# Kernel optimization log

Hardware: AMD Instinct MI355X
Metric: run time of the kernel (lower is better)

Reference implementation:

```python
import jax, jax.numpy as jnp
import numpy as np

DK, DV, NH = 512, 256, 8  # matches init_kwargs


def rel_to_abs(x):
    # x: (B, N, L, 2L-1) -> (B, N, L, L) via pad/reshape trick
    B, N, L, _ = x.shape
    x = jnp.pad(x, ((0, 0), (0, 0), (0, 0), (0, 1)))          # (B,N,L,2L)
    x = x.reshape(B, N, L * 2 * L)
    x = jnp.pad(x, ((0, 0), (0, 0), (0, L - 1)))
    x = x.reshape(B, N, L + 1, 2 * L - 1)
    return x[:, :, :L, L - 1:]


def relative_logits_1d(q, rel_k):
    # q: (B, nh, A, Wd, dkh); rel_k: (dkh, 2*Wd-1)
    B, nh, A, Wd, _ = q.shape
    rel = jnp.einsum('bnawc,cm->bnawm', q, rel_k)             # (B,nh,A,Wd,2Wd-1)
    rel = rel.reshape(B, nh * A, Wd, 2 * Wd - 1)
    rel = rel_to_abs(rel).reshape(B, nh, A, 1, Wd, Wd)
    return jnp.broadcast_to(rel, (B, nh, A, A, Wd, Wd))


def reference(x, w_qkv, w_conv, w_out, key_rel_h, key_rel_w):
    B, Cin, H, W = x.shape
    dkh, dvh = DK // NH, DV // NH
    L = H * W
    # 1x1 qkv projection (stride 1)
    qkv = jnp.einsum('bchw,oc->bohw', x, w_qkv)               # (B, 2dk+dv, H, W)
    q = qkv[:, :DK]
    k = qkv[:, DK:2 * DK]
    v = qkv[:, 2 * DK:]
    flat_q = q.reshape(B, NH, dkh, L) * (dkh ** -0.5)
    flat_k = k.reshape(B, NH, dkh, L)
    flat_v = v.reshape(B, NH, dvh, L)
    logits = jnp.einsum('bncs,bnct->bnst', flat_q, flat_k)     # (B,nh,L,L)
    # relative position logits (uses the already-scaled q, as in the torch code)
    qr = flat_q.reshape(B, NH, dkh, H, W).transpose(0, 1, 3, 4, 2)  # (B,nh,H,W,dkh)
    w_rel = relative_logits_1d(qr, key_rel_w)                  # (B,nh,H,H,W,W)
    h_rel = relative_logits_1d(qr.transpose(0, 1, 3, 2, 4), key_rel_h)  # (B,nh,W,W,H,H)
    h_rel = h_rel.transpose(0, 1, 2, 4, 3, 5).reshape(B, NH, L, L)
    w_rel = w_rel.transpose(0, 1, 4, 2, 5, 3).reshape(B, NH, L, L)
    logits = logits + h_rel + w_rel
    weights = jax.nn.softmax(logits, axis=-1)
    attn = jnp.einsum('bnst,bnct->bnsc', weights, flat_v)      # (B,nh,L,dvh)
    attn = attn.transpose(0, 1, 3, 2).reshape(B, DV, H, W)
    attn = jnp.einsum('bchw,oc->bohw', attn, w_out)            # 1x1 out_proj
    conv_out = jax.lax.conv_general_dilated(
        x, w_conv, window_strides=(1, 1), padding=[(1, 1), (1, 1)],
        dimension_numbers=('NCHW', 'OIHW', 'NCHW'))            # (B, out_c-dv, H, W)
    return jnp.concatenate([conv_out, attn], axis=1)


def setup_inputs() -> dict:
    key = jax.random.key(0)
    ks = jax.random.split(key, 6)
    H, W, Cin = 32, 32, 256
    return {
        'x': jax.random.normal(ks[0], (8, Cin, H, W), jnp.float32),
        'w_qkv': jax.random.normal(ks[1], (2 * DK + DV, Cin), jnp.float32) * 0.02,
        'w_conv': jax.random.normal(ks[2], (256, Cin, 3, 3), jnp.float32) * 0.02,
        'w_out': jax.random.normal(ks[3], (DV, DV), jnp.float32) * 0.02,
        'key_rel_h': DK ** -0.5 + jax.random.normal(ks[4], (DK // NH, 2 * H - 1), jnp.float32),
        'key_rel_w': DK ** -0.5 + jax.random.normal(ks[5], (DK // NH, 2 * W - 1), jnp.float32),
    }
```

## Files before the change

kernel.cpp:

```cpp
#include <hip/hip_runtime.h>
#include <cstddef>
#include <cstdint>

#define NB 8
#define CIN 256
#define LL 1024
#define DKC 512
#define DVC 256
#define XPSTRIDE 295936

typedef short short8 __attribute__((ext_vector_type(8)));
typedef float f32x4 __attribute__((ext_vector_type(4)));

__device__ __forceinline__ unsigned short f2bf(float f) {
  unsigned int u = __float_as_uint(f);
  u += 0x7fffu + ((u >> 16) & 1u);
  return (unsigned short)(u >> 16);
}
__device__ __forceinline__ float bf2f(unsigned short u) {
  return __uint_as_float(((unsigned int)u) << 16);
}

__global__ __launch_bounds__(256) void prep_weights(
    const float* __restrict__ wconv, const float* __restrict__ wqkv,
    const float* __restrict__ wout, const float* __restrict__ krh,
    const float* __restrict__ krw, unsigned short* __restrict__ wtap,
    unsigned short* __restrict__ wqbf, unsigned short* __restrict__ woutbf,
    unsigned short* __restrict__ relTh, unsigned short* __restrict__ relTw) {
  const int idx = blockIdx.x * 256 + threadIdx.x;
  if (idx < 589824) {
    const int tap = idx >> 16;
    const int rem = idx & 65535;
    wtap[idx] = f2bf(wconv[(size_t)rem * 9 + tap]);
  } else if (idx < 917504) {
    const int j = idx - 589824;
    const int o = j >> 8;
    const float sc = (o < DKC) ? 0.125f * 1.44269504088896f : 1.0f;
    wqbf[j] = f2bf(wqkv[j] * sc);
  } else if (idx < 983040) {
    const int j = idx - 917504;
    woutbf[j] = f2bf(wout[j]);
  } else {
    const int j = idx - 983040;
    const int tbl = j >> 12;
    const int rest = j & 4095;
    const int m = rest >> 6, c = rest & 63;
    const float* src = tbl ? krw : krh;
    unsigned short* dst = tbl ? relTw : relTh;
    const float v = (m < 63) ? src[c * 63 + m] : 0.f;
    dst[m * 64 + c] = f2bf(v);
  }
}

__global__ __launch_bounds__(256) void xpad_border(unsigned short* __restrict__ xTp) {
  const int idx = blockIdx.x * 256 + threadIdx.x;
  const int b = idx / 33792;
  const int rem = idx - b * 33792;
  const int pos = rem >> 8, c = rem & 255;
  int hp, wp;
  if (pos < 34) { hp = 0; wp = pos; }
  else if (pos < 68) { hp = 33; wp = pos - 34; }
  else if (pos < 100) { hp = pos - 68 + 1; wp = 0; }
  else { hp = pos - 100 + 1; wp = 33; }
  xTp[(size_t)b * XPSTRIDE + (hp * 34 + wp) * 256 + c] = 0;
}

__global__ __launch_bounds__(256) void xpad_interior(
    const float* __restrict__ x, unsigned short* __restrict__ xTp) {
  __shared__ float tile[64][65];
  const int st = blockIdx.x;
  const int b = blockIdx.y;
  const int s0 = st * 64;
  const int h0 = st * 2;
  const int tid = threadIdx.x;
  for (int cc = 0; cc < 4; ++cc) {
    const int c0 = cc * 64;
    {
      const int row = tid >> 2;
      const int j0 = (tid & 3) * 16;
#pragma unroll
      for (int k = 0; k < 4; ++k)
        *(float4*)&tile[row][j0 + k * 4] =
            *(const float4*)(x + ((size_t)(b * CIN + c0 + row)) * LL + s0 + j0 + k * 4);
    }
    __syncthreads();
    {
      const int sl = tid >> 2;
      const int cb = (tid & 3) * 16;
      unsigned short buf[16];
#pragma unroll
      for (int m = 0; m < 16; ++m) buf[m] = f2bf(tile[cb + m][sl]);
      const int hp = h0 + (sl >> 5) + 1;
      const int wp = (sl & 31) + 1;
      unsigned short* dst = xTp + (size_t)b * XPSTRIDE + (hp * 34 + wp) * 256 + c0 + cb;
      *(uint4*)dst = *(uint4*)&buf[0];
      *(uint4*)(dst + 8) = *(uint4*)&buf[8];
    }
    __syncthreads();
  }
}

__global__ __launch_bounds__(256) void qkv_mfma(
    const unsigned short* __restrict__ xTp, const unsigned short* __restrict__ wqbf,
    unsigned short* __restrict__ qbf, unsigned short* __restrict__ kbf,
    unsigned short* __restrict__ vbf) {
  __shared__ __align__(16) unsigned short as[64 * 64];
  __shared__ __align__(16) unsigned short bs[64 * 64];
  __shared__ float trans[64][65];
  const int tid = threadIdx.x;
  const int lane = tid & 63, w = tid >> 6;
  const int n16 = lane & 15, quad = lane >> 4;
  const int ot = blockIdx.x;
  const int st = blockIdx.y;
  const int b = blockIdx.z;
  const int o0 = ot * 64;
  const int s0 = st * 64;
  const int h0 = st * 2;
  const int trow = tid >> 3, ck = tid & 7;

  const unsigned short* xb = xTp + (size_t)b * XPSTRIDE;
  const unsigned short* wt = wqbf + (size_t)o0 * 256;
  const int wpos = (trow & 31) + 1;

  f32x4 acc[4];
#pragma unroll
  for (int nt = 0; nt < 4; ++nt) acc[nt] = (f32x4){0.f, 0.f, 0.f, 0.f};

  uint4 ra0, ra1, rb0, rb1;
  {
    ra0 = *(const uint4*)(wt + (size_t)trow * 256 + ck * 8);
    ra1 = *(const uint4*)(wt + (size_t)(trow + 32) * 256 + ck * 8);
    rb0 = *(const uint4*)(xb + (size_t)((h0 + 1) * 34 + wpos) * 256 + ck * 8);
    rb1 = *(const uint4*)(xb + (size_t)((h0 + 2) * 34 + wpos) * 256 + ck * 8);
  }
#pragma unroll
  for (int kc = 0; kc < 4; ++kc) {
    __syncthreads();
    *(uint4*)&as[trow * 64 + ((ck ^ (trow & 7)) * 8)] = ra0;
    *(uint4*)&as[(trow + 32) * 64 + ((ck ^ (trow & 7)) * 8)] = ra1;
    *(uint4*)&bs[trow * 64 + ((ck ^ (trow & 7)) * 8)] = rb0;
    *(uint4*)&bs[(trow + 32) * 64 + ((ck ^ (trow & 7)) * 8)] = rb1;
    __syncthreads();
    if (kc < 3) {
      const int c0 = (kc + 1) * 64;
      ra0 = *(const uint4*)(wt + (size_t)trow * 256 + c0 + ck * 8);
      ra1 = *(const uint4*)(wt + (size_t)(trow + 32) * 256 + c0 + ck * 8);
      rb0 = *(const uint4*)(xb + (size_t)((h0 + 1) * 34 + wpos) * 256 + c0 + ck * 8);
      rb1 = *(const uint4*)(xb + (size_t)((h0 + 2) * 34 + wpos) * 256 + c0 + ck * 8);
    }
    short8 a0 = *(const short8*)&as[(w * 16 + n16) * 64 + ((quad ^ (n16 & 7)) * 8)];
    short8 a1 = *(const short8*)&as[(w * 16 + n16) * 64 + (((quad + 4) ^ (n16 & 7)) * 8)];
#pragma unroll
    for (int nt = 0; nt < 4; ++nt) {
      short8 b0 = *(const short8*)&bs[(nt * 16 + n16) * 64 + ((quad ^ (n16 & 7)) * 8)];
      short8 b1 = *(const short8*)&bs[(nt * 16 + n16) * 64 + (((quad + 4) ^ (n16 & 7)) * 8)];
      acc[nt] = __builtin_amdgcn_mfma_f32_16x16x32_bf16(a0, b0, acc[nt], 0, 0, 0);
      acc[nt] = __builtin_amdgcn_mfma_f32_16x16x32_bf16(a1, b1, acc[nt], 0, 0, 0);
    }
  }
  __syncthreads();
#pragma unroll
  for (int nt = 0; nt < 4; ++nt)
#pragma unroll
    for (int reg = 0; reg < 4; ++reg)
      trans[w * 16 + quad * 4 + reg][nt * 16 + n16] = acc[nt][reg];
  __syncthreads();
  const int sl = tid >> 2;
  const int cseg = (tid & 3) * 16;
  unsigned short buf[16];
  if (ot < 16) {
#pragma unroll
    for (int m = 0; m < 16; ++m) buf[m] = f2bf(trans[cseg + m][sl]);
    unsigned short* dst;
    int head;
    if (ot < 8) { dst = qbf; head = ot; }
    else { dst = kbf; head = ot - 8; }
    const size_t base = (((size_t)(b * 8 + head)) * LL + s0 + sl) * 64 + cseg;
    *(uint4*)(dst + base) = *(uint4*)&buf[0];
    *(uint4*)(dst + base + 8) = *(uint4*)&buf[8];
  } else {
#pragma unroll
    for (int m = 0; m < 16; ++m) buf[m] = f2bf(trans[sl][cseg + m]);
    unsigned short* dst = vbf + ((size_t)b * DVC + (ot - 16) * 64 + sl) * LL + s0 + cseg;
    *(uint4*)dst = *(uint4*)&buf[0];
    *(uint4*)(dst + 8) = *(uint4*)&buf[8];
  }
}

__global__ __launch_bounds__(256) void conv_mfma(
    const unsigned short* __restrict__ xTp, const unsigned short* __restrict__ wtap,
    float* __restrict__ out) {
  __shared__ __align__(16) unsigned short as[64 * 64];
  __shared__ __align__(16) unsigned short bs[64 * 64];
  const int tid = threadIdx.x;
  const int lane = tid & 63, w = tid >> 6;
  const int n16 = lane & 15, quad = lane >> 4;
  const int ot = blockIdx.x;
  const int st = blockIdx.y;
  const int b = blockIdx.z;
  const int s0 = st * 64;
  const int h0 = st * 2;
  const int trow = tid >> 3;
  const int ck = tid & 7;

  const unsigned short* xb = xTp + (size_t)b * XPSTRIDE;
  const unsigned short* wbase = wtap + (size_t)(ot * 64) * 256;

  f32x4 acc[4];
#pragma unroll
  for (int nt = 0; nt < 4; ++nt) acc[nt] = (f32x4){0.f, 0.f, 0.f, 0.f};

  uint4 ra0, ra1, rb0, rb1;
  auto loadtile = [&](int it) {
    const int tap = it >> 2;
    const int c0 = (it & 3) * 64;
    const int dh = tap / 3 - 1;
    const int dw = tap - (tap / 3) * 3 - 1;
    const unsigned short* wt = wbase + (size_t)tap * 65536;
    ra0 = *(const uint4*)(wt + (size_t)trow * 256 + c0 + ck * 8);
    ra1 = *(const uint4*)(wt + (size_t)(trow + 32) * 256 + c0 + ck * 8);
    const int wp = (trow & 31) + dw + 1;
    rb0 = *(const uint4*)(xb + (size_t)((h0 + dh + 1) * 34 + wp) * 256 + c0 + ck * 8);
    rb1 = *(const uint4*)(xb + (size_t)((h0 + dh + 2) * 34 + wp) * 256 + c0 + ck * 8);
  };
  loadtile(0);
  for (int it = 0; it < 36; ++it) {
    __syncthreads();
    *(uint4*)&as[trow * 64 + ((ck ^ (trow & 7)) * 8)] = ra0;
    *(uint4*)&as[(trow + 32) * 64 + ((ck ^ (trow & 7)) * 8)] = ra1;
    *(uint4*)&bs[trow * 64 + ((ck ^ (trow & 7)) * 8)] = rb0;
    *(uint4*)&bs[(trow + 32) * 64 + ((ck ^ (trow & 7)) * 8)] = rb1;
    __syncthreads();
    if (it < 35) loadtile(it + 1);
    short8 a0 = *(const short8*)&as[(w * 16 + n16) * 64 + ((quad ^ (n16 & 7)) * 8)];
    short8 a1 = *(const short8*)&as[(w * 16 + n16) * 64 + (((quad + 4) ^ (n16 & 7)) * 8)];
#pragma unroll
    for (int nt = 0; nt < 4; ++nt) {
      short8 b0 = *(const short8*)&bs[(nt * 16 + n16) * 64 + ((quad ^ (n16 & 7)) * 8)];
      short8 b1 = *(const short8*)&bs[(nt * 16 + n16) * 64 + (((quad + 4) ^ (n16 & 7)) * 8)];
      acc[nt] = __builtin_amdgcn_mfma_f32_16x16x32_bf16(a0, b0, acc[nt], 0, 0, 0);
      acc[nt] = __builtin_amdgcn_mfma_f32_16x16x32_bf16(a1, b1, acc[nt], 0, 0, 0);
    }
  }
#pragma unroll
  for (int nt = 0; nt < 4; ++nt)
#pragma unroll
    for (int reg = 0; reg < 4; ++reg)
      out[((size_t)b * 512 + ot * 64 + w * 16 + quad * 4 + reg) * LL + s0 + nt * 16 + n16] =
          acc[nt][reg];
}

__global__ __launch_bounds__(256, 4) void attn_kernel(
    const unsigned short* __restrict__ qbf, const unsigned short* __restrict__ kbf,
    const unsigned short* __restrict__ vbf, const unsigned short* __restrict__ relTh,
    const unsigned short* __restrict__ relTw, unsigned short* __restrict__ abf) {
  __shared__ __align__(16) char smem[28672];
  unsigned short* ks = (unsigned short*)smem;
  unsigned short* vs = (unsigned short*)(smem + 8192);
  unsigned short* ps = (unsigned short*)(smem + 12288);
  unsigned short* rwtT = (unsigned short*)(smem + 20480);
  float* obuf = (float*)smem;

  const int tid = threadIdx.x;
  const int lane = tid & 63, w = tid >> 6;
  const int n16 = lane & 15, quad = lane >> 4;
  const int blk = blockIdx.x;
  const int bn = blk & 63, qb = blk >> 6;
  const int n = bn & 7, b = bn >> 3;
  const int s0 = qb * 64;
  const int aa = 2 * qb + (w >> 1);
  const int pb = (w & 1) * 16;

  const unsigned short* qbase = qbf + ((size_t)(b * 8 + n)) * LL * 64;
  const unsigned short* kbase = kbf + ((size_t)(b * 8 + n)) * LL * 64;
  const unsigned short* vbase = vbf + ((size_t)(b * 8 + n)) * 32 * LL;

  const int ck = tid & 7;
  const int trow = tid >> 3;

  uint4 pk0 = *(const uint4*)(kbase + trow * 64 + ck * 8);
  uint4 pk1 = *(const uint4*)(kbase + (trow + 32) * 64 + ck * 8);
  uint4 pv = *(const uint4*)(vbase + (size_t)trow * LL + ck * 8);

  {
    const int sT = (pb + n16) * 32 + aa;
    short8 ra0 = *(const short8*)(qbase + (size_t)sT * 64 + quad * 8);
    short8 ra1 = *(const short8*)(qbase + (size_t)sT * 64 + 32 + quad * 8);
#pragma unroll
    for (int tbl = 0; tbl < 2; ++tbl) {
      const unsigned short* rel = tbl ? relTh : relTw;
      f32x4 acc[4];
#pragma unroll
      for (int mt = 0; mt < 4; ++mt) acc[mt] = (f32x4){0.f, 0.f, 0.f, 0.f};
#pragma unroll
      for (int mt = 0; mt < 4; ++mt) {
        short8 b0 = *(const short8*)(rel + (mt * 16 + n16) * 64 + quad * 8);
        short8 b1 = *(const short8*)(rel + (mt * 16 + n16) * 64 + 32 + quad * 8);
        acc[mt] = __builtin_amdgcn_mfma_f32_16x16x32_bf16(ra0, b0, acc[mt], 0, 0, 0);
        acc[mt] = __builtin_amdgcn_mfma_f32_16x16x32_bf16(ra1, b1, acc[mt], 0, 0, 0);
      }
      if (tbl == 0) {
#pragma unroll
        for (int mt = 0; mt < 4; ++mt)
#pragma unroll
          for (int reg = 0; reg < 4; ++reg)
            rwtT[(mt * 16 + n16) * 64 +
                 ((w * 16 + quad * 4 + reg) ^ ((n16 & 7) * 8))] = f2bf(acc[mt][reg]);
      } else {
#pragma unroll
        for (int mt = 0; mt < 4; ++mt)
#pragma unroll
          for (int reg = 0; reg < 4; ++reg)
            ps[(w * 16 + quad * 4 + reg) * 64 + mt * 16 + n16] = f2bf(acc[mt][reg]);
      }
    }
  }
  short8 qf0 = *(const short8*)(qbase + (size_t)(s0 + w * 16 + n16) * 64 + quad * 8);
  short8 qf1 = *(const short8*)(qbase + (size_t)(s0 + w * 16 + n16) * 64 + 32 + quad * 8);
  __syncthreads();
  float rhreg[2][4];
#pragma unroll
  for (int tt1 = 0; tt1 < 2; ++tt1)
#pragma unroll
    for (int reg = 0; reg < 4; ++reg) {
      const int iL = quad * 4 + reg;
      rhreg[tt1][reg] = bf2f(ps[(w * 16 + iL) * 64 + tt1 * 16 + n16 + 31 - pb - iL]);
    }

  float lacc[4] = {0.f, 0.f, 0.f, 0.f};
  f32x4 oacc[2];
  oacc[0] = (f32x4){0.f, 0.f, 0.f, 0.f};
  oacc[1] = (f32x4){0.f, 0.f, 0.f, 0.f};

  unsigned short* psw = ps + w * 1024;
  const int rb = w * 16 + quad * 4;

  for (int kt64 = 0; kt64 < 16; ++kt64) {
    const int t0 = kt64 * 64;
    __syncthreads();
    *(uint4*)&ks[trow * 64 + ((ck ^ (trow & 7)) * 8)] = pk0;
    *(uint4*)&ks[(trow + 32) * 64 + ((ck ^ (trow & 7)) * 8)] = pk1;
    *(uint4*)&vs[trow * 64 + ((ck ^ (trow & 7)) * 8)] = pv;
    __syncthreads();
    if (kt64 < 15) {
      const unsigned short* kg = kbase + (size_t)(t0 + 64) * 64;
      pk0 = *(const uint4*)(kg + trow * 64 + ck * 8);
      pk1 = *(const uint4*)(kg + (trow + 32) * 64 + ck * 8);
      pv = *(const uint4*)(vbase + (size_t)trow * LL + t0 + 64 + ck * 8);
    }

    f32x4 sacc[4];
#pragma unroll
    for (int tt = 0; tt < 4; ++tt) sacc[tt] = (f32x4){0.f, 0.f, 0.f, 0.f};
#pragma unroll
    for (int tt = 0; tt < 4; ++tt) {
      short8 kb0 = *(const short8*)&ks[(tt * 16 + n16) * 64 + ((quad ^ (n16 & 7)) * 8)];
      short8 kb1 = *(const short8*)&ks[(tt * 16 + n16) * 64 + (((quad + 4) ^ (n16 & 7)) * 8)];
      sacc[tt] = __builtin_amdgcn_mfma_f32_16x16x32_bf16(qf0, kb0, sacc[tt], 0, 0, 0);
      sacc[tt] = __builtin_amdgcn_mfma_f32_16x16x32_bf16(qf1, kb1, sacc[tt], 0, 0, 0);
    }
    float rwv[2][4];
#pragma unroll
    for (int h = 0; h < 2; ++h) {
      const int mw = (t0 >> 5) + h - aa + 31;
      const ushort4 rw4 = *(const ushort4*)&rwtT[mw * 64 + (rb ^ ((mw & 7) * 8))];
      rwv[h][0] = bf2f(rw4.x); rwv[h][1] = bf2f(rw4.y);
      rwv[h][2] = bf2f(rw4.z); rwv[h][3] = bf2f(rw4.w);
    }
#pragma unroll
    for (int tt = 0; tt < 4; ++tt)
#pragma unroll
      for (int reg = 0; reg < 4; ++reg) {
        const float e =
            __builtin_amdgcn_exp2f(sacc[tt][reg] + rwv[tt >> 1][reg] + rhreg[tt & 1][reg]);
        lacc[reg] += e;
        const int r = quad * 4 + reg;
        psw[r * 64 + (((tt * 2 + (n16 >> 3)) ^ (r & 7)) * 8) + (n16 & 7)] =
            (unsigned short)(__float_as_uint(e) >> 16);
      }
    __asm__ volatile("s_waitcnt lgkmcnt(0)" ::: "memory");
#pragma unroll
    for (int kt = 0; kt < 2; ++kt) {
      short8 pa = *(const short8*)&psw[n16 * 64 + (((quad + 4 * kt) ^ (n16 & 7)) * 8)];
#pragma unroll
      for (int ct = 0; ct < 2; ++ct) {
        short8 vb = *(const short8*)&vs[(ct * 16 + n16) * 64 + (((quad + 4 * kt) ^ (n16 & 7)) * 8)];
        oacc[ct] = __builtin_amdgcn_mfma_f32_16x16x32_bf16(pa, vb, oacc[ct], 0, 0, 0);
      }
    }
  }
  float linv[4];
#pragma unroll
  for (int reg = 0; reg < 4; ++reg) {
    float l = lacc[reg];
#pragma unroll
    for (int m = 1; m < 16; m <<= 1) l += __shfl_xor(l, m, 16);
    linv[reg] = 1.0f / l;
  }
  __syncthreads();
#pragma unroll
  for (int ct = 0; ct < 2; ++ct)
#pragma unroll
    for (int reg = 0; reg < 4; ++reg)
      obuf[(w * 16 + quad * 4 + reg) * 33 + ct * 16 + n16] = oacc[ct][reg] * linv[reg];
  __syncthreads();
  {
    const int row = tid >> 2;
    const int cseg = (tid & 3) * 8;
    unsigned short buf8[8];
#pragma unroll
    for (int m = 0; m < 8; ++m) buf8[m] = f2bf(obuf[row * 33 + cseg + m]);
    *(uint4*)(abf + (((size_t)b * LL) + s0 + row) * 256 + n * 32 + cseg) = *(uint4*)&buf8[0];
  }
}

__global__ __launch_bounds__(256) void proj_mfma(
    const unsigned short* __restrict__ abf, const unsigned short* __restrict__ woutbf,
    float* __restrict__ out) {
  __shared__ __align__(16) unsigned short as[64 * 64];
  __shared__ __align__(16) unsigned short bs[64 * 64];
  const int tid = threadIdx.x;
  const int lane = tid & 63, w = tid >> 6;
  const int n16 = lane & 15, quad = lane >> 4;
  const int ot = blockIdx.x;
  const int st = blockIdx.y;
  const int b = blockIdx.z;
  const int o0 = ot * 64;
  const int s0 = st * 64;
  const int trow = tid >> 3, ck = tid & 7;

  const unsigned short* ab = abf + ((size_t)b * LL + s0) * 256;
  const unsigned short* wt = woutbf + (size_t)o0 * 256;

  f32x4 acc[4];
#pragma unroll
  for (int nt = 0; nt < 4; ++nt) acc[nt] = (f32x4){0.f, 0.f, 0.f, 0.f};

  uint4 ra0, ra1, rb0, rb1;
  ra0 = *(const uint4*)(wt + (size_t)trow * 256 + ck * 8);
  ra1 = *(const uint4*)(wt + (size_t)(trow + 32) * 256 + ck * 8);
  rb0 = *(const uint4*)(ab + (size_t)trow * 256 + ck * 8);
  rb1 = *(const uint4*)(ab + (size_t)(trow + 32) * 256 + ck * 8);
#pragma unroll
  for (int kc = 0; kc < 4; ++kc) {
    __syncthreads();
    *(uint4*)&as[trow * 64 + ((ck ^ (trow & 7)) * 8)] = ra0;
    *(uint4*)&as[(trow + 32) * 64 + ((ck ^ (trow & 7)) * 8)] = ra1;
    *(uint4*)&bs[trow * 64 + ((ck ^ (trow & 7)) * 8)] = rb0;
    *(uint4*)&bs[(trow + 32) * 64 + ((ck ^ (trow & 7)) * 8)] = rb1;
    __syncthreads();
    if (kc < 3) {
      const int c0 = (kc + 1) * 64;
      ra0 = *(const uint4*)(wt + (size_t)trow * 256 + c0 + ck * 8);
      ra1 = *(const uint4*)(wt + (size_t)(trow + 32) * 256 + c0 + ck * 8);
      rb0 = *(const uint4*)(ab + (size_t)trow * 256 + c0 + ck * 8);
      rb1 = *(const uint4*)(ab + (size_t)(trow + 32) * 256 + c0 + ck * 8);
    }
    short8 a0 = *(const short8*)&as[(w * 16 + n16) * 64 + ((quad ^ (n16 & 7)) * 8)];
    short8 a1 = *(const short8*)&as[(w * 16 + n16) * 64 + (((quad + 4) ^ (n16 & 7)) * 8)];
#pragma unroll
    for (int nt = 0; nt < 4; ++nt) {
      short8 b0 = *(const short8*)&bs[(nt * 16 + n16) * 64 + ((quad ^ (n16 & 7)) * 8)];
      short8 b1 = *(const short8*)&bs[(nt * 16 + n16) * 64 + (((quad + 4) ^ (n16 & 7)) * 8)];
      acc[nt] = __builtin_amdgcn_mfma_f32_16x16x32_bf16(a0, b0, acc[nt], 0, 0, 0);
      acc[nt] = __builtin_amdgcn_mfma_f32_16x16x32_bf16(a1, b1, acc[nt], 0, 0, 0);
    }
  }
#pragma unroll
  for (int nt = 0; nt < 4; ++nt)
#pragma unroll
    for (int reg = 0; reg < 4; ++reg)
      out[((size_t)b * 512 + 256 + o0 + w * 16 + quad * 4 + reg) * LL + s0 + nt * 16 + n16] =
          acc[nt][reg];
}

extern "C" void kernel_launch(void* const* d_in, const int* in_sizes, int n_in,
                              void* d_out, int out_size, void* d_ws, size_t ws_size,
                              hipStream_t stream) {
  const float* x     = (const float*)d_in[0];
  const float* wqkv  = (const float*)d_in[1];
  const float* wconv = (const float*)d_in[2];
  const float* wout  = (const float*)d_in[3];
  const float* krh   = (const float*)d_in[4];
  const float* krw   = (const float*)d_in[5];
  float* out = (float*)d_out;

  unsigned short* qbf = (unsigned short*)d_ws;
  unsigned short* kbf = qbf + (size_t)NB * 8 * LL * 64;
  unsigned short* vbf = kbf + (size_t)NB * 8 * LL * 64;
  unsigned short* abf = vbf + (size_t)NB * DVC * LL;
  unsigned short* relTh = abf + (size_t)NB * LL * DVC;
  unsigned short* relTw = relTh + 4096;
  unsigned short* xTp = relTw + 4096;
  unsigned short* wtap = xTp + (size_t)NB * XPSTRIDE;
  unsigned short* wqbf = wtap + 589824;
  unsigned short* woutbf = wqbf + 327680;

  prep_weights<<<dim3(3872), 256, 0, stream>>>(wconv, wqkv, wout, krh, krw,
                                               wtap, wqbf, woutbf, relTh, relTw);
  xpad_border<<<dim3(1056), 256, 0, stream>>>(xTp);
  xpad_interior<<<dim3(16, 8), 256, 0, stream>>>(x, xTp);
  qkv_mfma<<<dim3(20, 16, NB), 256, 0, stream>>>(xTp, wqbf, qbf, kbf, vbf);
  conv_mfma<<<dim3(4, 16, NB), 256, 0, stream>>>(xTp, wtap, out);
  attn_kernel<<<dim3(1024), 256, 0, stream>>>(qbf, kbf, vbf, relTh, relTw, abf);
  proj_mfma<<<dim3(4, 16, NB), 256, 0, stream>>>(abf, woutbf, out);
}
```

Baseline: 160.8 us.

## Merge conv and qkv launches, fold border zeroing, double attention rows per block

Folds the xpad border zeroing into prep_weights and merges the conv and qkv GEMMs into one launch, where block index selects the path, which removes launches and lets the two GEMMs run concurrently. The attention kernel now handles 128 query rows per block instead of 64, reusing each K/V tile loaded into shared memory across two row sets. In exchange it uses more shared memory and registers (launch bounds drop to 2 blocks per CU) and launches half as many blocks, which may reduce occupancy and load balance. Mixing 36-iteration conv blocks with 4-iteration qkv blocks in one grid can leave the merged launch imbalanced.

```diff
diff --git a/kernel.cpp b/kernel.cpp
--- a/kernel.cpp
+++ b/kernel.cpp
@@ -26,7 +26,8 @@
     const float* __restrict__ wout, const float* __restrict__ krh,
     const float* __restrict__ krw, unsigned short* __restrict__ wtap,
     unsigned short* __restrict__ wqbf, unsigned short* __restrict__ woutbf,
-    unsigned short* __restrict__ relTh, unsigned short* __restrict__ relTw) {
+    unsigned short* __restrict__ relTh, unsigned short* __restrict__ relTw,
+    unsigned short* __restrict__ xTp) {
   const int idx = blockIdx.x * 256 + threadIdx.x;
   if (idx < 589824) {
     const int tap = idx >> 16;
@@ -40,7 +41,7 @@
   } else if (idx < 983040) {
     const int j = idx - 917504;
     woutbf[j] = f2bf(wout[j]);
-  } else {
+  } else if (idx < 991232) {
     const int j = idx - 983040;
     const int tbl = j >> 12;
     const int rest = j & 4095;
@@ -49,20 +50,18 @@
     unsigned short* dst = tbl ? relTw : relTh;
     const float v = (m < 63) ? src[c * 63 + m] : 0.f;
     dst[m * 64 + c] = f2bf(v);
-  }
-}
-
-__global__ __launch_bounds__(256) void xpad_border(unsigned short* __restrict__ xTp) {
-  const int idx = blockIdx.x * 256 + threadIdx.x;
-  const int b = idx / 33792;
-  const int rem = idx - b * 33792;
-  const int pos = rem >> 8, c = rem & 255;
-  int hp, wp;
-  if (pos < 34) { hp = 0; wp = pos; }
-  else if (pos < 68) { hp = 33; wp = pos - 34; }
-  else if (pos < 100) { hp = pos - 68 + 1; wp = 0; }
-  else { hp = pos - 100 + 1; wp = 33; }
-  xTp[(size_t)b * XPSTRIDE + (hp * 34 + wp) * 256 + c] = 0;
+  } else {
+    const int j2 = idx - 991232;
+    const int b = j2 / 33792;
+    const int rem = j2 - b * 33792;
+    const int pos = rem >> 8, c = rem & 255;
+    int hp, wp;
+    if (pos < 34) { hp = 0; wp = pos; }
+    else if (pos < 68) { hp = 33; wp = pos - 34; }
+    else if (pos < 100) { hp = pos - 68 + 1; wp = 0; }
+    else { hp = pos - 100 + 1; wp = 33; }
+    xTp[(size_t)b * XPSTRIDE + (hp * 34 + wp) * 256 + c] = 0;
+  }
 }
 
 __global__ __launch_bounds__(256) void xpad_interior(
@@ -100,8 +99,9 @@
   }
 }
 
-__global__ __launch_bounds__(256) void qkv_mfma(
-    const unsigned short* __restrict__ xTp, const unsigned short* __restrict__ wqbf,
+__global__ __launch_bounds__(256) void convqkv_mfma(
+    const unsigned short* __restrict__ xTp, const unsigned short* __restrict__ wtap,
+    const unsigned short* __restrict__ wqbf, float* __restrict__ out,
     unsigned short* __restrict__ qbf, unsigned short* __restrict__ kbf,
     unsigned short* __restrict__ vbf) {
   __shared__ __align__(16) unsigned short as[64 * 64];
@@ -110,166 +110,144 @@
   const int tid = threadIdx.x;
   const int lane = tid & 63, w = tid >> 6;
   const int n16 = lane & 15, quad = lane >> 4;
-  const int ot = blockIdx.x;
+  const int otg = blockIdx.x;
   const int st = blockIdx.y;
   const int b = blockIdx.z;
-  const int o0 = ot * 64;
   const int s0 = st * 64;
   const int h0 = st * 2;
   const int trow = tid >> 3, ck = tid & 7;
 
   const unsigned short* xb = xTp + (size_t)b * XPSTRIDE;
-  const unsigned short* wt = wqbf + (size_t)o0 * 256;
-  const int wpos = (trow & 31) + 1;
 
   f32x4 acc[4];
 #pragma unroll
   for (int nt = 0; nt < 4; ++nt) acc[nt] = (f32x4){0.f, 0.f, 0.f, 0.f};
 
-  uint4 ra0, ra1, rb0, rb1;
-  {
+  if (otg < 4) {
+    const int ot = otg;
+    const unsigned short* wbase = wtap + (size_t)(ot * 64) * 256;
+    uint4 ra0, ra1, rb0, rb1;
+    auto loadtile = [&](int it) {
+      const int tap = it >> 2;
+      const int c0 = (it & 3) * 64;
+      const int dh = tap / 3 - 1;
+      const int dw = tap - (tap / 3) * 3 - 1;
+      const unsigned short* wt = wbase + (size_t)tap * 65536;
+      ra0 = *(const uint4*)(wt + (size_t)trow * 256 + c0 + ck * 8);
+      ra1 = *(const uint4*)(wt + (size_t)(trow + 32) * 256 + c0 + ck * 8);
+      const int wp = (trow & 31) + dw + 1;
+      rb0 = *(const uint4*)(xb + (size_t)((h0 + dh + 1) * 34 + wp) * 256 + c0 + ck * 8);
+      rb1 = *(const uint4*)(xb + (size_t)((h0 + dh + 2) * 34 + wp) * 256 + c0 + ck * 8);
+    };
+    loadtile(0);
+    for (int it = 0; it < 36; ++it) {
+      __syncthreads();
+      *(uint4*)&as[trow * 64 + ((ck ^ (trow & 7)) * 8)] = ra0;
+      *(uint4*)&as[(trow + 32) * 64 + ((ck ^ (trow & 7)) * 8)] = ra1;
+      *(uint4*)&bs[trow * 64 + ((ck ^ (trow & 7)) * 8)] = rb0;
+      *(uint4*)&bs[(trow + 32) * 64 + ((ck ^ (trow & 7)) * 8)] = rb1;
+      __syncthreads();
+      if (it < 35) loadtile(it + 1);
+      short8 a0 = *(const short8*)&as[(w * 16 + n16) * 64 + ((quad ^ (n16 & 7)) * 8)];
+      short8 a1 = *(const short8*)&as[(w * 16 + n16) * 64 + (((quad + 4) ^ (n16 & 7)) * 8)];
+#pragma unroll
+      for (int nt = 0; nt < 4; ++nt) {
+        short8 b0 = *(const short8*)&bs[(nt * 16 + n16) * 64 + ((quad ^ (n16 & 7)) * 8)];
+        short8 b1 = *(const short8*)&bs[(nt * 16 + n16) * 64 + (((quad + 4) ^ (n16 & 7)) * 8)];
+        acc[nt] = __builtin_amdgcn_mfma_f32_16x16x32_bf16(a0, b0, acc[nt], 0, 0, 0);
+        acc[nt] = __builtin_amdgcn_mfma_f32_16x16x32_bf16(a1, b1, acc[nt], 0, 0, 0);
+      }
+    }
+#pragma unroll
+    for (int nt = 0; nt < 4; ++nt)
+#pragma unroll
+      for (int reg = 0; reg < 4; ++reg)
+        out[((size_t)b * 512 + ot * 64 + w * 16 + quad * 4 + reg) * LL + s0 + nt * 16 + n16] =
+            acc[nt][reg];
+  } else {
+    const int ot = otg - 4;
+    const unsigned short* wt = wqbf + (size_t)(ot * 64) * 256;
+    const int wpos = (trow & 31) + 1;
+    uint4 ra0, ra1, rb0, rb1;
     ra0 = *(const uint4*)(wt + (size_t)trow * 256 + ck * 8);
     ra1 = *(const uint4*)(wt + (size_t)(trow + 32) * 256 + ck * 8);
     rb0 = *(const uint4*)(xb + (size_t)((h0 + 1) * 34 + wpos) * 256 + ck * 8);
     rb1 = *(const uint4*)(xb + (size_t)((h0 + 2) * 34 + wpos) * 256 + ck * 8);
-  }
-#pragma unroll
-  for (int kc = 0; kc < 4; ++kc) {
-    __syncthreads();
-    *(uint4*)&as[trow * 64 + ((ck ^ (trow & 7)) * 8)] = ra0;
-    *(uint4*)&as[(trow + 32) * 64 + ((ck ^ (trow & 7)) * 8)] = ra1;
-    *(uint4*)&bs[trow * 64 + ((ck ^ (trow & 7)) * 8)] = rb0;
-    *(uint4*)&bs[(trow + 32) * 64 + ((ck ^ (trow & 7)) * 8)] = rb1;
-    __syncthreads();
-    if (kc < 3) {
-      const int c0 = (kc + 1) * 64;
-      ra0 = *(const uint4*)(wt + (size_t)trow * 256 + c0 + ck * 8);
-      ra1 = *(const uint4*)(wt + (size_t)(trow + 32) * 256 + c0 + ck * 8);
-      rb0 = *(const uint4*)(xb + (size_t)((h0 + 1) * 34 + wpos) * 256 + c0 + ck * 8);
-      rb1 = *(const uint4*)(xb + (size_t)((h0 + 2) * 34 + wpos) * 256 + c0 + ck * 8);
-    }
-    short8 a0 = *(const short8*)&as[(w * 16 + n16) * 64 + ((quad ^ (n16 & 7)) * 8)];
-    short8 a1 = *(const short8*)&as[(w * 16 + n16) * 64 + (((quad + 4) ^ (n16 & 7)) * 8)];
-#pragma unroll
-    for (int nt = 0; nt < 4; ++nt) {
-      short8 b0 = *(const short8*)&bs[(nt * 16 + n16) * 64 + ((quad ^ (n16 & 7)) * 8)];
-      short8 b1 = *(const short8*)&bs[(nt * 16 + n16) * 64 + (((quad + 4) ^ (n16 & 7)) * 8)];
-      acc[nt] = __builtin_amdgcn_mfma_f32_16x16x32_bf16(a0, b0, acc[nt], 0, 0, 0);
-      acc[nt] = __builtin_amdgcn_mfma_f32_16x16x32_bf16(a1, b1, acc[nt], 0, 0, 0);
-    }
-  }
-  __syncthreads();
-#pragma unroll
-  for (int nt = 0; nt < 4; ++nt)
-#pragma unroll
-    for (int reg = 0; reg < 4; ++reg)
-      trans[w * 16 + quad * 4 + reg][nt * 16 + n16] = acc[nt][reg];
-  __syncthreads();
-  const int sl = tid >> 2;
-  const int cseg = (tid & 3) * 16;
-  unsigned short buf[16];
-  if (ot < 16) {
-#pragma unroll
-    for (int m = 0; m < 16; ++m) buf[m] = f2bf(trans[cseg + m][sl]);
-    unsigned short* dst;
-    int head;
-    if (ot < 8) { dst = qbf; head = ot; }
-    else { dst = kbf; head = ot - 8; }
-    const size_t base = (((size_t)(b * 8 + head)) * LL + s0 + sl) * 64 + cseg;
-    *(uint4*)(dst + base) = *(uint4*)&buf[0];
-    *(uint4*)(dst + base + 8) = *(uint4*)&buf[8];
-  } else {
-#pragma unroll
-    for (int m = 0; m < 16; ++m) buf[m] = f2bf(trans[sl][cseg + m]);
-    unsigned short* dst = vbf + ((size_t)b * DVC + (ot - 16) * 64 + sl) * LL + s0 + cseg;
-    *(uint4*)dst = *(uint4*)&buf[0];
-    *(uint4*)(dst + 8) = *(uint4*)&buf[8];
-  }
-}
-
-__global__ __launch_bounds__(256) void conv_mfma(
-    const unsigned short* __restrict__ xTp, const unsigned short* __restrict__ wtap,
-    float* __restrict__ out) {
-  __shared__ __align__(16) unsigned short as[64 * 64];
-  __shared__ __align__(16) unsigned short bs[64 * 64];
-  const int tid = threadIdx.x;
-  const int lane = tid & 63, w = tid >> 6;
-  const int n16 = lane & 15, quad = lane >> 4;
-  const int ot = blockIdx.x;
-  const int st = blockIdx.y;
-  const int b = blockIdx.z;
-  const int s0 = st * 64;
-  const int h0 = st * 2;
-  const int trow = tid >> 3;
-  const int ck = tid & 7;
-
-  const unsigned short* xb = xTp + (size_t)b * XPSTRIDE;
-  const unsigned short* wbase = wtap + (size_t)(ot * 64) * 256;
-
-  f32x4 acc[4];
-#pragma unroll
-  for (int nt = 0; nt < 4; ++nt) acc[nt] = (f32x4){0.f, 0.f, 0.f, 0.f};
-
-  uint4 ra0, ra1, rb0, rb1;
-  auto loadtile = [&](int it) {
-    const int tap = it >> 2;
-    const int c0 = (it & 3) * 64;
-    const int dh = tap / 3 - 1;
-    const int dw = tap - (tap / 3) * 3 - 1;
-    const unsigned short* wt = wbase + (size_t)tap * 65536;
-    ra0 = *(const uint4*)(wt + (size_t)trow * 256 + c0 + ck * 8);
-    ra1 = *(const uint4*)(wt + (size_t)(trow + 32) * 256 + c0 + ck * 8);
-    const int wp = (trow & 31) + dw + 1;
-    rb0 = *(const uint4*)(xb + (size_t)((h0 + dh + 1) * 34 + wp) * 256 + c0 + ck * 8);
-    rb1 = *(const uint4*)(xb + (size_t)((h0 + dh + 2) * 34 + wp) * 256 + c0 + ck * 8);
-  };
-  loadtile(0);
-  for (int it = 0; it < 36; ++it) {
-    __syncthreads();
-    *(uint4*)&as[trow * 64 + ((ck ^ (trow & 7)) * 8)] = ra0;
-    *(uint4*)&as[(trow + 32) * 64 + ((ck ^ (trow & 7)) * 8)] = ra1;
-    *(uint4*)&bs[trow * 64 + ((ck ^ (trow & 7)) * 8)] = rb0;
-    *(uint4*)&bs[(trow + 32) * 64 + ((ck ^ (trow & 7)) * 8)] = rb1;
-    __syncthreads();
-    if (it < 35) loadtile(it + 1);
-    short8 a0 = *(const short8*)&as[(w * 16 + n16) * 64 + ((quad ^ (n16 & 7)) * 8)];
-    short8 a1 = *(const short8*)&as[(w * 16 + n16) * 64 + (((quad + 4) ^ (n16 & 7)) * 8)];
-#pragma unroll
-    for (int nt = 0; nt < 4; ++nt) {
-      short8 b0 = *(const short8*)&bs[(nt * 16 + n16) * 64 + ((quad ^ (n16 & 7)) * 8)];
-      short8 b1 = *(const short8*)&bs[(nt * 16 + n16) * 64 + (((quad + 4) ^ (n16 & 7)) * 8)];
-      acc[nt] = __builtin_amdgcn_mfma_f32_16x16x32_bf16(a0, b0, acc[nt], 0, 0, 0);
-      acc[nt] = __builtin_amdgcn_mfma_f32_16x16x32_bf16(a1, b1, acc[nt], 0, 0, 0);
-    }
-  }
-#pragma unroll
-  for (int nt = 0; nt < 4; ++nt)
-#pragma unroll
-    for (int reg = 0; reg < 4; ++reg)
-      out[((size_t)b * 512 + ot * 64 + w * 16 + quad * 4 + reg) * LL + s0 + nt * 16 + n16] =
-          acc[nt][reg];
-}
-
-__global__ __launch_bounds__(256, 4) void attn_kernel(
+#pragma unroll
+    for (int kc = 0; kc < 4; ++kc) {
+      __syncthreads();
+      *(uint4*)&as[trow * 64 + ((ck ^ (trow & 7)) * 8)] = ra0;
+      *(uint4*)&as[(trow + 32) * 64 + ((ck ^ (trow & 7)) * 8)] = ra1;
+      *(uint4*)&bs[trow * 64 + ((ck ^ (trow & 7)) * 8)] = rb0;
+      *(uint4*)&bs[(trow + 32) * 64 + ((ck ^ (trow & 7)) * 8)] = rb1;
+      __syncthreads();
+      if (kc < 3) {
+        const int c0 = (kc + 1) * 64;
+        ra0 = *(const uint4*)(wt + (size_t)trow * 256 + c0 + ck * 8);
+        ra1 = *(const uint4*)(wt + (size_t)(trow + 32) * 256 + c0 + ck * 8);
+        rb0 = *(const uint4*)(xb + (size_t)((h0 + 1) * 34 + wpos) * 256 + c0 + ck * 8);
+        rb1 = *(const uint4*)(xb + (size_t)((h0 + 2) * 34 + wpos) * 256 + c0 + ck * 8);
+      }
+      short8 a0 = *(const short8*)&as[(w * 16 + n16) * 64 + ((quad ^ (n16 & 7)) * 8)];
+      short8 a1 = *(const short8*)&as[(w * 16 + n16) * 64 + (((quad + 4) ^ (n16 & 7)) * 8)];
+#pragma unroll
+      for (int nt = 0; nt < 4; ++nt) {
+        short8 b0 = *(const short8*)&bs[(nt * 16 + n16) * 64 + ((quad ^ (n16 & 7)) * 8)];
+        short8 b1 = *(const short8*)&bs[(nt * 16 + n16) * 64 + (((quad + 4) ^ (n16 & 7)) * 8)];
+        acc[nt] = __builtin_amdgcn_mfma_f32_16x16x32_bf16(a0, b0, acc[nt], 0, 0, 0);
+        acc[nt] = __builtin_amdgcn_mfma_f32_16x16x32_bf16(a1, b1, acc[nt], 0, 0, 0);
+      }
+    }
+    __syncthreads();
+#pragma unroll
+    for (int nt = 0; nt < 4; ++nt)
+#pragma unroll
+      for (int reg = 0; reg < 4; ++reg)
+        trans[w * 16 + quad * 4 + reg][nt * 16 + n16] = acc[nt][reg];
+    __syncthreads();
+    const int sl = tid >> 2;
+    const int cseg = (tid & 3) * 16;
+    unsigned short buf[16];
+    if (ot < 16) {
+#pragma unroll
+      for (int m = 0; m < 16; ++m) buf[m] = f2bf(trans[cseg + m][sl]);
+      unsigned short* dst;
+      int head;
+      if (ot < 8) { dst = qbf; head = ot; }
+      else { dst = kbf; head = ot - 8; }
+      const size_t base = (((size_t)(b * 8 + head)) * LL + s0 + sl) * 64 + cseg;
+      *(uint4*)(dst + base) = *(uint4*)&buf[0];
+      *(uint4*)(dst + base + 8) = *(uint4*)&buf[8];
+    } else {
+#pragma unroll
+      for (int m = 0; m < 16; ++m) buf[m] = f2bf(trans[sl][cseg + m]);
+      unsigned short* dst = vbf + ((size_t)b * DVC + (ot - 16) * 64 + sl) * LL + s0 + cseg;
+      *(uint4*)dst = *(uint4*)&buf[0];
+      *(uint4*)(dst + 8) = *(uint4*)&buf[8];
+    }
+  }
+}
+
+__global__ __launch_bounds__(256, 2) void attn_kernel(
     const unsigned short* __restrict__ qbf, const unsigned short* __restrict__ kbf,
     const unsigned short* __restrict__ vbf, const unsigned short* __restrict__ relTh,
     const unsigned short* __restrict__ relTw, unsigned short* __restrict__ abf) {
-  __shared__ __align__(16) char smem[28672];
+  __shared__ __align__(16) char smem[45056];
   unsigned short* ks = (unsigned short*)smem;
   unsigned short* vs = (unsigned short*)(smem + 8192);
   unsigned short* ps = (unsigned short*)(smem + 12288);
-  unsigned short* rwtT = (unsigned short*)(smem + 20480);
+  unsigned short* rwtT = (unsigned short*)(smem + 28672);
   float* obuf = (float*)smem;
 
   const int tid = threadIdx.x;
   const int lane = tid & 63, w = tid >> 6;
   const int n16 = lane & 15, quad = lane >> 4;
   const int blk = blockIdx.x;
-  const int bn = blk & 63, qb = blk >> 6;
+  const int bn = blk & 63, qt = blk >> 6;
   const int n = bn & 7, b = bn >> 3;
-  const int s0 = qb * 64;
-  const int aa = 2 * qb + (w >> 1);
+  const int s0 = qt * 128;
   const int pb = (w & 1) * 16;
+  const int aar[2] = {4 * qt + (w >> 1), 4 * qt + 2 + (w >> 1)};
 
   const unsigned short* qbase = qbf + ((size_t)(b * 8 + n)) * LL * 64;
   const unsigned short* kbase = kbf + ((size_t)(b * 8 + n)) * LL * 64;
@@ -282,7 +260,9 @@
   uint4 pk1 = *(const uint4*)(kbase + (trow + 32) * 64 + ck * 8);
   uint4 pv = *(const uint4*)(vbase + (size_t)trow * LL + ck * 8);
 
-  {
+#pragma unroll
+  for (int rs = 0; rs < 2; ++rs) {
+    const int aa = aar[rs];
     const int sT = (pb + n16) * 32 + aa;
     short8 ra0 = *(const short8*)(qbase + (size_t)sT * 64 + quad * 8);
     short8 ra1 = *(const short8*)(qbase + (size_t)sT * 64 + 32 + quad * 8);
@@ -304,36 +284,45 @@
         for (int mt = 0; mt < 4; ++mt)
 #pragma unroll
           for (int reg = 0; reg < 4; ++reg)
-            rwtT[(mt * 16 + n16) * 64 +
-                 ((w * 16 + quad * 4 + reg) ^ ((n16 & 7) * 8))] = f2bf(acc[mt][reg]);
+            rwtT[(mt * 16 + n16) * 128 +
+                 ((rs * 64 + w * 16 + quad * 4 + reg) ^ ((n16 & 7) * 8))] = f2bf(acc[mt][reg]);
       } else {
 #pragma unroll
         for (int mt = 0; mt < 4; ++mt)
 #pragma unroll
           for (int reg = 0; reg < 4; ++reg)
-            ps[(w * 16 + quad * 4 + reg) * 64 + mt * 16 + n16] = f2bf(acc[mt][reg]);
-      }
-    }
-  }
-  short8 qf0 = *(const short8*)(qbase + (size_t)(s0 + w * 16 + n16) * 64 + quad * 8);
-  short8 qf1 = *(const short8*)(qbase + (size_t)(s0 + w * 16 + n16) * 64 + 32 + quad * 8);
+            ps[(rs * 64 + w * 16 + quad * 4 + reg) * 64 + mt * 16 + n16] = f2bf(acc[mt][reg]);
+      }
+    }
+  }
+  short8 qf[2][2];
+#pragma unroll
+  for (int rs = 0; rs < 2; ++rs) {
+    const size_t qrow = (size_t)(s0 + rs * 64 + w * 16 + n16) * 64;
+    qf[rs][0] = *(const short8*)(qbase + qrow + quad * 8);
+    qf[rs][1] = *(const short8*)(qbase + qrow + 32 + quad * 8);
+  }
   __syncthreads();
-  float rhreg[2][4];
-#pragma unroll
-  for (int tt1 = 0; tt1 < 2; ++tt1)
-#pragma unroll
-    for (int reg = 0; reg < 4; ++reg) {
-      const int iL = quad * 4 + reg;
-      rhreg[tt1][reg] = bf2f(ps[(w * 16 + iL) * 64 + tt1 * 16 + n16 + 31 - pb - iL]);
-    }
-
-  float lacc[4] = {0.f, 0.f, 0.f, 0.f};
-  f32x4 oacc[2];
-  oacc[0] = (f32x4){0.f, 0.f, 0.f, 0.f};
-  oacc[1] = (f32x4){0.f, 0.f, 0.f, 0.f};
-
-  unsigned short* psw = ps + w * 1024;
-  const int rb = w * 16 + quad * 4;
+  float rhreg[2][2][4];
+#pragma unroll
+  for (int rs = 0; rs < 2; ++rs)
+#pragma unroll
+    for (int tt1 = 0; tt1 < 2; ++tt1)
+#pragma unroll
+      for (int reg = 0; reg < 4; ++reg) {
+        const int iL = quad * 4 + reg;
+        rhreg[rs][tt1][reg] =
+            bf2f(ps[(rs * 64 + w * 16 + iL) * 64 + tt1 * 16 + n16 + 31 - pb - iL]);
+      }
+
+  float lacc[2][4] = {};
+  f32x4 oacc[2][2];
+#pragma unroll
+  for (int rs = 0; rs < 2; ++rs)
+#pragma unroll
+    for (int ct = 0; ct < 2; ++ct) oacc[rs][ct] = (f32x4){0.f, 0.f, 0.f, 0.f};
+
+  const int rbq = w * 16 + quad * 4;
 
   for (int kt64 = 0; kt64 < 16; ++kt64) {
     const int t0 = kt64 * 64;
@@ -349,68 +338,91 @@
       pv = *(const uint4*)(vbase + (size_t)trow * LL + t0 + 64 + ck * 8);
     }
 
-    f32x4 sacc[4];
-#pragma unroll
-    for (int tt = 0; tt < 4; ++tt) sacc[tt] = (f32x4){0.f, 0.f, 0.f, 0.f};
+    f32x4 sacc[2][4];
+#pragma unroll
+    for (int rs = 0; rs < 2; ++rs)
+#pragma unroll
+      for (int tt = 0; tt < 4; ++tt) sacc[rs][tt] = (f32x4){0.f, 0.f, 0.f, 0.f};
 #pragma unroll
     for (int tt = 0; tt < 4; ++tt) {
       short8 kb0 = *(const short8*)&ks[(tt * 16 + n16) * 64 + ((quad ^ (n16 & 7)) * 8)];
       short8 kb1 = *(const short8*)&ks[(tt * 16 + n16) * 64 + (((quad + 4) ^ (n16 & 7)) * 8)];
-      sacc[tt] = __builtin_amdgcn_mfma_f32_16x16x32_bf16(qf0, kb0, sacc[tt], 0, 0, 0);
-      sacc[tt] = __builtin_amdgcn_mfma_f32_16x16x32_bf16(qf1, kb1, sacc[tt], 0, 0, 0);
-    }
-    float rwv[2][4];
-#pragma unroll
-    for (int h = 0; h < 2; ++h) {
-      const int mw = (t0 >> 5) + h - aa + 31;
-      const ushort4 rw4 = *(const ushort4*)&rwtT[mw * 64 + (rb ^ ((mw & 7) * 8))];
-      rwv[h][0] = bf2f(rw4.x); rwv[h][1] = bf2f(rw4.y);
-      rwv[h][2] = bf2f(rw4.z); rwv[h][3] = bf2f(rw4.w);
-    }
-#pragma unroll
-    for (int tt = 0; tt < 4; ++tt)
-#pragma unroll
-      for (int reg = 0; reg < 4; ++reg) {
-        const float e =
-            __builtin_amdgcn_exp2f(sacc[tt][reg] + rwv[tt >> 1][reg] + rhreg[tt & 1][reg]);
-        lacc[reg] += e;
-        const int r = quad * 4 + reg;
-        psw[r * 64 + (((tt * 2 + (n16 >> 3)) ^ (r & 7)) * 8) + (n16 & 7)] =
-            (unsigned short)(__float_as_uint(e) >> 16);
-      }
+#pragma unroll
+      for (int rs = 0; rs < 2; ++rs) {
+        sacc[rs][tt] = __builtin_amdgcn_mfma_f32_16x16x32_bf16(qf[rs][0], kb0, sacc[rs][tt], 0, 0, 0);
+        sacc[rs][tt] = __builtin_amdgcn_mfma_f32_16x16x32_bf16(qf[rs][1], kb1, sacc[rs][tt], 0, 0, 0);
+      }
+    }
+    float rwv[2][2][4];
+#pragma unroll
+    for (int rs = 0; rs < 2; ++rs)
+#pragma unroll
+      for (int h = 0; h < 2; ++h) {
+        const int mw = (t0 >> 5) + h - aar[rs] + 31;
+        const ushort4 rw4 =
+            *(const ushort4*)&rwtT[mw * 128 + ((rs * 64 + rbq) ^ ((mw & 7) * 8))];
+        rwv[rs][h][0] = bf2f(rw4.x); rwv[rs][h][1] = bf2f(rw4.y);
+        rwv[rs][h][2] = bf2f(rw4.z); rwv[rs][h][3] = bf2f(rw4.w);
+      }
+#pragma unroll
+    for (int rs = 0; rs < 2; ++rs)
+#pragma unroll
+      for (int tt = 0; tt < 4; ++tt)
+#pragma unroll
+        for (int reg = 0; reg < 4; ++reg) {
+          const float e = __builtin_amdgcn_exp2f(sacc[rs][tt][reg] + rwv[rs][tt >> 1][reg] +
+                                                 rhreg[rs][tt & 1][reg]);
+          lacc[rs][reg] += e;
+          const int r = quad * 4 + reg;
+          ps[(rs * 64 + w * 16 + r) * 64 + (((tt * 2 + (n16 >> 3)) ^ (r & 7)) * 8) + (n16 & 7)] =
+              (unsigned short)(__float_as_uint(e) >> 16);
+        }
     __asm__ volatile("s_waitcnt lgkmcnt(0)" ::: "memory");
 #pragma unroll
     for (int kt = 0; kt < 2; ++kt) {
-      short8 pa = *(const short8*)&psw[n16 * 64 + (((quad + 4 * kt) ^ (n16 & 7)) * 8)];
+      short8 pa[2];
+#pragma unroll
+      for (int rs = 0; rs < 2; ++rs)
+        pa[rs] = *(const short8*)&ps[(rs * 64 + w * 16 + n16) * 64 +
+                                     (((quad + 4 * kt) ^ (n16 & 7)) * 8)];
 #pragma unroll
       for (int ct = 0; ct < 2; ++ct) {
         short8 vb = *(const short8*)&vs[(ct * 16 + n16) * 64 + (((quad + 4 * kt) ^ (n16 & 7)) * 8)];
-        oacc[ct] = __builtin_amdgcn_mfma_f32_16x16x32_bf16(pa, vb, oacc[ct], 0, 0, 0);
-      }
-    }
-  }
-  float linv[4];
-#pragma unroll
-  for (int reg = 0; reg < 4; ++reg) {
-    float l = lacc[reg];
-#pragma unroll
-    for (int m = 1; m < 16; m <<= 1) l += __shfl_xor(l, m, 16);
-    linv[reg] = 1.0f / l;
-  }
+#pragma unroll
+        for (int rs = 0; rs < 2; ++rs)
+          oacc[rs][ct] = __builtin_amdgcn_mfma_f32_16x16x32_bf16(pa[rs], vb, oacc[rs][ct], 0, 0, 0);
+      }
+    }
+  }
+  float linv[2][4];
+#pragma unroll
+  for (int rs = 0; rs < 2; ++rs)
+#pragma unroll
+    for (int reg = 0; reg < 4; ++reg) {
+      float l = lacc[rs][reg];
+#pragma unroll
+      for (int m = 1; m < 16; m <<= 1) l += __shfl_xor(l, m, 16);
+      linv[rs][reg] = 1.0f / l;
+    }
   __syncthreads();
 #pragma unroll
-  for (int ct = 0; ct < 2; ++ct)
-#pragma unroll
-    for (int reg = 0; reg < 4; ++reg)
-      obuf[(w * 16 + quad * 4 + reg) * 33 + ct * 16 + n16] = oacc[ct][reg] * linv[reg];
+  for (int rs = 0; rs < 2; ++rs)
+#pragma unroll
+    for (int ct = 0; ct < 2; ++ct)
+#pragma unroll
+      for (int reg = 0; reg < 4; ++reg)
+        obuf[(rs * 64 + w * 16 + quad * 4 + reg) * 33 + ct * 16 + n16] =
+            oacc[rs][ct][reg] * linv[rs][reg];
   __syncthreads();
   {
-    const int row = tid >> 2;
-    const int cseg = (tid & 3) * 8;
-    unsigned short buf8[8];
-#pragma unroll
-    for (int m = 0; m < 8; ++m) buf8[m] = f2bf(obuf[row * 33 + cseg + m]);
-    *(uint4*)(abf + (((size_t)b * LL) + s0 + row) * 256 + n * 32 + cseg) = *(uint4*)&buf8[0];
+    const int row = tid >> 1;
+    const int cseg = (tid & 1) * 16;
+    unsigned short buf16[16];
+#pragma unroll
+    for (int m = 0; m < 16; ++m) buf16[m] = f2bf(obuf[row * 33 + cseg + m]);
+    unsigned short* dst = abf + (((size_t)b * LL) + s0 + row) * 256 + n * 32 + cseg;
+    *(uint4*)dst = *(uint4*)&buf16[0];
+    *(uint4*)(dst + 8) = *(uint4*)&buf16[8];
   }
 }
 
@@ -496,12 +508,10 @@
   unsigned short* wqbf = wtap + 589824;
   unsigned short* woutbf = wqbf + 327680;
 
-  prep_weights<<<dim3(3872), 256, 0, stream>>>(wconv, wqkv, wout, krh, krw,
-                                               wtap, wqbf, woutbf, relTh, relTw);
-  xpad_border<<<dim3(1056), 256, 0, stream>>>(xTp);
+  prep_weights<<<dim3(4928), 256, 0, stream>>>(wconv, wqkv, wout, krh, krw,
+                                               wtap, wqbf, woutbf, relTh, relTw, xTp);
   xpad_interior<<<dim3(16, 8), 256, 0, stream>>>(x, xTp);
-  qkv_mfma<<<dim3(20, 16, NB), 256, 0, stream>>>(xTp, wqbf, qbf, kbf, vbf);
-  conv_mfma<<<dim3(4, 16, NB), 256, 0, stream>>>(xTp, wtap, out);
-  attn_kernel<<<dim3(1024), 256, 0, stream>>>(qbf, kbf, vbf, relTh, relTw, abf);
+  convqkv_mfma<<<dim3(24, 16, NB), 256, 0, stream>>>(xTp, wtap, wqbf, out, qbf, kbf, vbf);
+  attn_kernel<<<dim3(512), 256, 0, stream>>>(qbf, kbf, vbf, relTh, relTw, abf);
   proj_mfma<<<dim3(4, 16, NB), 256, 0, stream>>>(abf, woutbf, out);
 }
```

After: 180.1 us. 1.12x slower.
